# Kernel tuning notes

Hardware: AMD Instinct MI355X
Metric: run time of the kernel (lower is better)

Reference implementation:

```python
import jax, jax.numpy as jnp
import numpy as np

B, N = 16, 512            # graphs, atoms per graph
F_DIM, H, D = 128, 64, 16  # feature_dim, hidden_dim, far_source_dim
CUT, GROWTH = 5.0, 2.0
NS, NT = 3, 2
MULT = GROWTH ** NS        # default far_max_radius_multiplier = 8
EMAX = CUT * MULT          # 40.0
TOT = NS + NT              # 5 shells total
SF = D + 3                 # 19 per-shell features
SE_IN = TOT * SF           # 95
EH_IN = 4 * D + SE_IN      # 159
N_RBF = 8
BOUNDS = [(5.0, 10.0), (10.0, 20.0), (20.0, 40.0), (40.0, 80.0), (80.0, float('inf'))]


def ln(x, g, b):
    m = x.mean(-1, keepdims=True)
    v = x.var(-1, keepdims=True)
    return (x - m) / jnp.sqrt(v + 1e-5) * g + b


def setup_inputs() -> dict:
    key = jax.random.key(0)
    ks = jax.random.split(key, 16)
    W = lambda k, i, o: jax.random.normal(k, (i, o), jnp.float32) / np.sqrt(i)
    inp = {}
    inp['x'] = jax.random.normal(ks[0], (B * N, F_DIM), jnp.float32)
    inp['pos'] = jax.random.uniform(ks[1], (B * N, 3), jnp.float32) * 80.0
    inp['batch'] = jnp.repeat(jnp.arange(B, dtype=jnp.int32), N)
    inp['num_graphs'] = B
    inp['in_ln_g'] = jnp.ones(F_DIM); inp['in_ln_b'] = jnp.zeros(F_DIM)
    inp['src_w1'] = W(ks[2], F_DIM, H); inp['src_b1'] = jnp.zeros(H)
    inp['src_w2'] = W(ks[3], H, D);     inp['src_b2'] = jnp.zeros(D)
    inp['src_ln_g'] = jnp.ones(D); inp['src_ln_b'] = jnp.zeros(D)
    inp['se_ln_g'] = jnp.ones(SE_IN); inp['se_ln_b'] = jnp.zeros(SE_IN)
    inp['se_w1'] = W(ks[4], SE_IN, H); inp['se_b1'] = jnp.zeros(H)
    inp['se_w2'] = W(ks[5], H, D);     inp['se_b2'] = jnp.zeros(D)
    inp['eh_ln_g'] = jnp.ones(EH_IN); inp['eh_ln_b'] = jnp.zeros(EH_IN)
    inp['eh_w1'] = W(ks[6], EH_IN, H); inp['eh_b1'] = jnp.zeros(H)
    inp['eh_w2'] = W(ks[7], H, 1);     inp['eh_b2'] = jnp.zeros(1)
    inp['k_screen'] = jnp.float32(-8.0)
    inp['kg_w1'] = W(ks[8], N_RBF + 2, 32); inp['kg_b1'] = jnp.zeros(32)
    inp['kg_w2'] = jnp.zeros((32, 1)); inp['kg_b2'] = jnp.zeros(1)  # zero-init per source
    inp['far_gate'] = jnp.float32(0.2)
    inp['energy_scale'] = jnp.float32(0.0)
    return inp


def reference(x, pos, batch, num_graphs, in_ln_g, in_ln_b, src_w1, src_b1, src_w2, src_b2,
              src_ln_g, src_ln_b, se_ln_g, se_ln_b, se_w1, se_b1, se_w2, se_b2,
              eh_ln_g, eh_ln_b, eh_w1, eh_b1, eh_w2, eh_b2,
              k_screen, kg_w1, kg_b1, kg_w2, kg_b2, far_gate, energy_scale):
    M = x.shape[0]
    n = M // num_graphs
    # per-atom source features
    h = ln(x, in_ln_g, in_ln_b)
    src = jax.nn.silu(h @ src_w1 + src_b1) @ src_w2 + src_b2
    src = ln(src, src_ln_g, src_ln_b)
    # graph-wise neutralization (subtract per-graph mean)
    gsum = jax.ops.segment_sum(src, batch, num_segments=num_graphs)
    cnt = jax.ops.segment_sum(jnp.ones((M, 1), x.dtype), batch, num_segments=num_graphs)
    src = src - (gsum / jnp.maximum(cnt, 1.0))[batch]
    # pairwise distances per graph
    p = pos.reshape(num_graphs, n, 3)
    s = src.reshape(num_graphs, n, D)
    diff = p[:, :, None, :] - p[:, None, :, :]
    d = jnp.sqrt((diff * diff).sum(-1) + 1e-12)  # [B,n,n]
    not_self = ~jnp.eye(n, dtype=bool)[None]
    # physical kernel with learned RBF gate
    screening = jax.nn.softplus(k_screen)
    base = jnp.exp(-screening * d) / jnp.maximum(d, 1e-6)
    centers = jnp.linspace(CUT, EMAX, N_RBF)
    spacing = (EMAX - CUT) / (N_RBF - 1)
    gamma = 1.0 / (spacing * spacing)
    dc = d[..., None]
    rbf = jnp.exp(-gamma * (dc - centers) ** 2)
    gin = jnp.concatenate([dc / CUT, dc / EMAX, rbf], -1)
    gate = 1.0 + jnp.tanh(jax.nn.silu(gin @ kg_w1 + kg_b1) @ kg_w2 + kg_b2)[..., 0]
    ker = base * gate
    # shell statistics: kernel-weighted mean source, count, mean_r, rms_r per shell
    feats = []
    for lo, up in BOUNDS:
        m = (d >= lo) & not_self
        if np.isfinite(up):
            m = m & (d < up)
        mf = m.astype(x.dtype)
        c = mf.sum(-1)
        denom = jnp.maximum(c, 1.0)
        mean = jnp.einsum('bij,bjc->bic', ker * mf, s) / denom[..., None]
        mr = (mf * d).sum(-1) / denom
        rr = jnp.sqrt((mf * d * d).sum(-1) / denom + 1e-12)
        feats.append(jnp.concatenate([mean, c[..., None], mr[..., None], rr[..., None]], -1))
    shell = jnp.concatenate(feats, -1).reshape(M, SE_IN)  # [M, 95]
    emb = jax.nn.silu(ln(shell, se_ln_g, se_ln_b) @ se_w1 + se_b1) @ se_w2 + se_b2
    ein = jnp.concatenate([src, emb, src * emb, src - emb, shell], -1)  # [M, 159]
    pa = (jax.nn.silu(ln(ein, eh_ln_g, eh_ln_b) @ eh_w1 + eh_b1) @ eh_w2 + eh_b2)[..., 0]
    pa = pa * jnp.tanh(far_gate) * jnp.exp(energy_scale)
    return jax.ops.segment_sum(pa, batch, num_segments=num_graphs)  # per-graph energies [B]
```

## Files before the change

kernel.cpp:

```cpp
#include <hip/hip_runtime.h>
#include <hip/hip_bf16.h>
#include <math.h>

#define B_G   16
#define N_A   512
#define M_AT  8192
#define FD    128
#define HD    64
#define DD    16
#define SEIN  95
#define EHIN  159
#define NLUT  512
#define DMAXF 140.0f

__device__ __forceinline__ float silu_f(float z) { return z / (1.f + __expf(-z)); }

__global__ __launch_bounds__(128) void k_front(
    const float* __restrict__ x,
    const float* __restrict__ g, const float* __restrict__ bb,
    const float* __restrict__ w1, const float* __restrict__ b1,
    const float* __restrict__ w2, const float* __restrict__ b2,
    const float* __restrict__ lng, const float* __restrict__ lnb,
    const float* __restrict__ k_screen,
    const float* __restrict__ kg_w1, const float* __restrict__ kg_b1,
    const float* __restrict__ kg_w2, const float* __restrict__ kg_b2,
    float* __restrict__ srcout, float* __restrict__ partials,
    float2* __restrict__ lut, float* __restrict__ out) {
  int t = threadIdx.x;

  __shared__ __align__(16) float xns[2][FD][5];
  __shared__ __align__(16) float hb[2][HD][5];
  __shared__ float psum[2][16];
  __shared__ float w1l[320], b1l[32], w2l[32];

  if (blockIdx.x >= 1024) {
    int lb = blockIdx.x - 1024;
    if (lb == 0 && t < B_G) out[t] = 0.f;
    for (int idx = t; idx < 320; idx += 128) w1l[idx] = kg_w1[idx];
    if (t < 32) { b1l[t] = kg_b1[t]; w2l[t] = kg_w2[t]; }
    __syncthreads();
    int i = lb * 128 + t;
    float step = DMAXF / (float)(NLUT - 1);
    float ksv = k_screen[0];
    float screening = fmaxf(ksv, 0.f) + log1pf(expf(-fabsf(ksv)));
    float b2v = kg_b2[0];
    float vals[2];
#pragma unroll
    for (int e = 0; e < 2; ++e) {
      int ii = min(i + e, NLUT - 1);
      float d = (float)ii * step;
      float base = expf(-screening * d) / fmaxf(d, 1e-6f);
      float gin[10];
      gin[0] = d * (1.f / 5.0f);
      gin[1] = d * (1.f / 40.0f);
#pragma unroll
      for (int kk = 0; kk < 8; ++kk) {
        float u = d - (5.0f + 5.0f * (float)kk);
        gin[2 + kk] = expf(-(1.f / 25.f) * u * u);
      }
      float accv = 0.f;
      for (int h = 0; h < 32; ++h) {
        float z = b1l[h];
#pragma unroll
        for (int kk = 0; kk < 10; ++kk) z += gin[kk] * w1l[kk * 32 + h];
        accv += silu_f(z) * w2l[h];
      }
      vals[e] = base * (1.f + tanhf(accv + b2v));
    }
    lut[i] = make_float2(vals[0], vals[1] - vals[0]);
    return;
  }

  int wave = t >> 6, lane = t & 63;
  int a = lane >> 4;
  int s = lane & 15;
  int aBase = blockIdx.x * 8 + wave * 4;

  float xr[8];
  {
    const float4* xp = (const float4*)(x + (size_t)(aBase + a) * FD + s * 8);
    float4 v0 = xp[0], v1 = xp[1];
    xr[0]=v0.x; xr[1]=v0.y; xr[2]=v0.z; xr[3]=v0.w;
    xr[4]=v1.x; xr[5]=v1.y; xr[6]=v1.z; xr[7]=v1.w;
  }
  float sm_ = 0.f;
#pragma unroll
  for (int i = 0; i < 8; ++i) sm_ += xr[i];
  sm_ += __shfl_xor(sm_, 1); sm_ += __shfl_xor(sm_, 2);
  sm_ += __shfl_xor(sm_, 4); sm_ += __shfl_xor(sm_, 8);
  float m = sm_ * (1.f / 128.f);
  float v2 = 0.f;
#pragma unroll
  for (int i = 0; i < 8; ++i) { float d = xr[i] - m; v2 += d * d; }
  v2 += __shfl_xor(v2, 1); v2 += __shfl_xor(v2, 2);
  v2 += __shfl_xor(v2, 4); v2 += __shfl_xor(v2, 8);
  float inv = rsqrtf(v2 * (1.f / 128.f) + 1e-5f);
#pragma unroll
  for (int i = 0; i < 8; ++i) {
    int k = s * 8 + i;
    xns[wave][k][a] = (xr[i] - m) * inv * g[k] + bb[k];
  }

  float acc[4] = {0.f, 0.f, 0.f, 0.f};
#pragma unroll 8
  for (int k = 0; k < FD; ++k) {
    float4 wv = ((const float4*)(w1 + (size_t)k * HD))[s];
    float xa = xns[wave][k][a];
    acc[0] += wv.x * xa; acc[1] += wv.y * xa;
    acc[2] += wv.z * xa; acc[3] += wv.w * xa;
  }
  {
    float4 bv = ((const float4*)b1)[s];
    hb[wave][s * 4 + 0][a] = silu_f(acc[0] + bv.x);
    hb[wave][s * 4 + 1][a] = silu_f(acc[1] + bv.y);
    hb[wave][s * 4 + 2][a] = silu_f(acc[2] + bv.z);
    hb[wave][s * 4 + 3][a] = silu_f(acc[3] + bv.w);
  }

  float e = 0.f;
#pragma unroll 8
  for (int k = 0; k < HD; ++k) e += hb[wave][k][a] * w2[k * DD + s];
  float val = e + b2[s];

  float smv = val;
  smv += __shfl_xor(smv, 1); smv += __shfl_xor(smv, 2);
  smv += __shfl_xor(smv, 4); smv += __shfl_xor(smv, 8);
  float mm = smv * (1.f / 16.f);
  float dv = val - mm;
  float vv = dv * dv;
  vv += __shfl_xor(vv, 1); vv += __shfl_xor(vv, 2);
  vv += __shfl_xor(vv, 4); vv += __shfl_xor(vv, 8);
  float iv = rsqrtf(vv * (1.f / 16.f) + 1e-5f);
  float ov = dv * iv * lng[s] + lnb[s];
  srcout[(size_t)(aBase + a) * DD + s] = ov;

  float lsum = ov;
  lsum += __shfl_xor(lsum, 16); lsum += __shfl_xor(lsum, 32);
  if (lane < 16) psum[wave][lane] = lsum;
  __syncthreads();
  if (t < 16) partials[(size_t)blockIdx.x * 16 + t] = psum[0][t] + psum[1][t];
}

__global__ __launch_bounds__(256) void k_pairs_tail(
    const float* __restrict__ pos, const float* __restrict__ src,
    const float2* __restrict__ lut, const float* __restrict__ partials,
    const float* __restrict__ se_ln_g, const float* __restrict__ se_ln_b,
    const float* __restrict__ se_w1, const float* __restrict__ se_b1,
    const float* __restrict__ se_w2, const float* __restrict__ se_b2,
    const float* __restrict__ eh_ln_g, const float* __restrict__ eh_ln_b,
    const float* __restrict__ eh_w1, const float* __restrict__ eh_b1,
    const float* __restrict__ eh_w2, const float* __restrict__ eh_b2,
    const float* __restrict__ far_gate, const float* __restrict__ energy_scale,
    float* __restrict__ out) {
  int gph = blockIdx.x >> 7;
  int blk = blockIdx.x & 127;
  int t = threadIdx.x, wave = t >> 6, lane = t & 63;
  int i_local = blk * 4 + wave;

  __shared__ __align__(16) float sp[N_A * 3];
  __shared__ __align__(16) float ss[N_A * DD];
  __shared__ __align__(16) float2 luts[NLUT];
  __shared__ float smean[16];
  __shared__ __align__(16) float einL[4][160];
  __shared__ __align__(16) float shnL[4][96];
  __shared__ __align__(16) float hbL[4][64];
  __shared__ float redv[4];

  for (int idx = t; idx < N_A * 3 / 4; idx += 256)
    ((float4*)sp)[idx] = ((const float4*)(pos + (size_t)gph * N_A * 3))[idx];
  for (int idx = t; idx < N_A * DD / 4; idx += 256)
    ((float4*)ss)[idx] = ((const float4*)(src + (size_t)gph * N_A * DD))[idx];
  if (t < NLUT / 2) ((float4*)luts)[t] = ((const float4*)lut)[t];
  if (t < 64) {
    int c = t & 15, grp = t >> 4;
    float sm = 0.f;
#pragma unroll
    for (int kk = 0; kk < 16; ++kk)
      sm += partials[(size_t)(gph * 64 + grp * 16 + kk) * 16 + c];
    sm += __shfl_xor(sm, 16); sm += __shfl_xor(sm, 32);
    if (t < 16) smean[c] = sm * (1.f / 512.f);
  }
  __syncthreads();

  int jlow = lane & 15, cq = lane >> 4;
  float px = sp[i_local * 3], py = sp[i_local * 3 + 1], pz = sp[i_local * 3 + 2];
  float accq[5][4] = {};
  float cnt[5] = {0,0,0,0,0}, sdv[5] = {0,0,0,0,0}, sdd[5] = {0,0,0,0,0}, swq[5] = {0,0,0,0,0};
  const float lscale = (float)(NLUT - 1) / DMAXF;

#pragma unroll 8
  for (int jj = 0; jj < 32; ++jj) {
    int j = jj * 16 + jlow;
    float dx = px - sp[j * 3], dy = py - sp[j * 3 + 1], dz = pz - sp[j * 3 + 2];
    float d2 = dx * dx + dy * dy + dz * dz + 1e-12f;
    float d = sqrtf(d2);
    bool valid = (j != i_local) && (d >= 5.0f);
    int tq = (d >= 10.f) + (d >= 20.f) + (d >= 40.f) + (d >= 80.f);
    float xq = d * lscale;
    int i0 = min((int)xq, NLUT - 2);
    float f = xq - (float)i0;
    float2 L = luts[i0];
    float w = valid ? (L.x + L.y * f) : 0.f;
    float dm = valid ? d : 0.f;
    float ddm = valid ? d * d : 0.f;
    float cm = valid ? 1.f : 0.f;
    float4 sv = *(const float4*)&ss[j * DD + cq * 4];
#pragma unroll
    for (int q = 0; q < 5; ++q) {
      bool mq = (tq == q);
      float wq = mq ? w : 0.f;
      accq[q][0] += wq * sv.x; accq[q][1] += wq * sv.y;
      accq[q][2] += wq * sv.z; accq[q][3] += wq * sv.w;
      cnt[q] += mq ? cm : 0.f;
      sdv[q] += mq ? dm : 0.f;
      sdd[q] += mq ? ddm : 0.f;
      swq[q] += wq;
    }
  }
#pragma unroll
  for (int q = 0; q < 5; ++q)
#pragma unroll
    for (int i = 0; i < 4; ++i) {
      float v = accq[q][i];
      v += __shfl_xor(v, 1); v += __shfl_xor(v, 2);
      v += __shfl_xor(v, 4); v += __shfl_xor(v, 8);
      accq[q][i] = v;
    }
#pragma unroll
  for (int q = 0; q < 5; ++q) {
#pragma unroll
    for (int o = 32; o > 0; o >>= 1) {
      cnt[q] += __shfl_xor(cnt[q], o);
      sdv[q] += __shfl_xor(sdv[q], o);
      sdd[q] += __shfl_xor(sdd[q], o);
      swq[q] += __shfl_xor(swq[q], o);
    }
    cnt[q] *= 0.25f; sdv[q] *= 0.25f; sdd[q] *= 0.25f; swq[q] *= 0.25f;
  }

  if (jlow == 0) {
#pragma unroll
    for (int q = 0; q < 5; ++q) {
      float denom = fmaxf(cnt[q], 1.f);
#pragma unroll
      for (int i = 0; i < 4; ++i) {
        int c = cq * 4 + i;
        einL[wave][64 + q * 19 + c] = (accq[q][i] - smean[c] * swq[q]) / denom;
      }
    }
  }
  if (lane < 5) {
    int q = lane;
    float denom = fmaxf(cnt[q], 1.f);
    einL[wave][64 + q * 19 + 16] = cnt[q];
    einL[wave][64 + q * 19 + 17] = sdv[q] / denom;
    einL[wave][64 + q * 19 + 18] = sqrtf(sdd[q] / denom + 1e-12f);
  }

  {
    float v0 = einL[wave][64 + lane];
    float v1 = (lane < 31) ? einL[wave][128 + lane] : 0.f;
    float s1 = v0 + v1, sq = v0 * v0 + v1 * v1;
#pragma unroll
    for (int o = 32; o > 0; o >>= 1) { s1 += __shfl_xor(s1, o); sq += __shfl_xor(sq, o); }
    float mn = s1 * (1.f / (float)SEIN);
    float var = sq * (1.f / (float)SEIN) - mn * mn;
    float invv = rsqrtf(var + 1e-5f);
    shnL[wave][lane] = (v0 - mn) * invv * se_ln_g[lane] + se_ln_b[lane];
    if (lane < 31)
      shnL[wave][64 + lane] = (v1 - mn) * invv * se_ln_g[64 + lane] + se_ln_b[64 + lane];
  }

  {
    float z = se_b1[lane];
#pragma unroll 5
    for (int k = 0; k < SEIN; ++k) z += shnL[wave][k] * se_w1[(size_t)k * HD + lane];
    hbL[wave][lane] = silu_f(z);
  }

  {
    int c = lane & 15, kq = lane >> 4;
    float e = 0.f;
#pragma unroll
    for (int i = 0; i < 16; ++i) {
      int k = kq * 16 + i;
      e += hbL[wave][k] * se_w2[k * DD + c];
    }
    e += __shfl_down(e, 32);
    e += __shfl_down(e, 16);
    if (lane < 16) {
      float ev = e + se_b2[lane];
      float svv = ss[i_local * DD + lane] - smean[lane];
      einL[wave][lane] = svv;
      einL[wave][16 + lane] = ev;
      einL[wave][32 + lane] = svv * ev;
      einL[wave][48 + lane] = svv - ev;
    }
  }

  {
    float u0 = einL[wave][lane];
    float u1 = einL[wave][64 + lane];
    float u2 = (lane < 31) ? einL[wave][128 + lane] : 0.f;
    float s1 = u0 + u1 + u2, sq = u0 * u0 + u1 * u1 + u2 * u2;
#pragma unroll
    for (int o = 32; o > 0; o >>= 1) { s1 += __shfl_xor(s1, o); sq += __shfl_xor(sq, o); }
    float mn = s1 * (1.f / (float)EHIN);
    float var = sq * (1.f / (float)EHIN) - mn * mn;
    float invv = rsqrtf(var + 1e-5f);
    einL[wave][lane] = (u0 - mn) * invv * eh_ln_g[lane] + eh_ln_b[lane];
    einL[wave][64 + lane] = (u1 - mn) * invv * eh_ln_g[64 + lane] + eh_ln_b[64 + lane];
    if (lane < 31)
      einL[wave][128 + lane] = (u2 - mn) * invv * eh_ln_g[128 + lane] + eh_ln_b[128 + lane];
  }

  {
    float z2 = eh_b1[lane];
#pragma unroll 3
    for (int k = 0; k < EHIN; ++k) z2 += einL[wave][k] * eh_w1[(size_t)k * HD + lane];
    float pa = silu_f(z2) * eh_w2[lane];
#pragma unroll
    for (int o = 32; o > 0; o >>= 1) pa += __shfl_xor(pa, o);
    if (lane == 0) redv[wave] = pa + eh_b2[0];
  }
  __syncthreads();
  if (t == 0) {
    float tot = redv[0] + redv[1] + redv[2] + redv[3];
    atomicAdd(&out[gph], tot * tanhf(far_gate[0]) * expf(energy_scale[0]));
  }
}

extern "C" void kernel_launch(void* const* d_in, const int* in_sizes, int n_in,
                              void* d_out, int out_size, void* d_ws, size_t ws_size,
                              hipStream_t stream) {
  const float* x         = (const float*)d_in[0];
  const float* pos       = (const float*)d_in[1];
  const float* in_ln_g   = (const float*)d_in[4];
  const float* in_ln_b   = (const float*)d_in[5];
  const float* src_w1    = (const float*)d_in[6];
  const float* src_b1    = (const float*)d_in[7];
  const float* src_w2    = (const float*)d_in[8];
  const float* src_b2    = (const float*)d_in[9];
  const float* src_ln_g  = (const float*)d_in[10];
  const float* src_ln_b  = (const float*)d_in[11];
  const float* se_ln_g   = (const float*)d_in[12];
  const float* se_ln_b   = (const float*)d_in[13];
  const float* se_w1     = (const float*)d_in[14];
  const float* se_b1     = (const float*)d_in[15];
  const float* se_w2     = (const float*)d_in[16];
  const float* se_b2     = (const float*)d_in[17];
  const float* eh_ln_g   = (const float*)d_in[18];
  const float* eh_ln_b   = (const float*)d_in[19];
  const float* eh_w1     = (const float*)d_in[20];
  const float* eh_b1     = (const float*)d_in[21];
  const float* eh_w2     = (const float*)d_in[22];
  const float* eh_b2     = (const float*)d_in[23];
  const float* k_screen  = (const float*)d_in[24];
  const float* kg_w1     = (const float*)d_in[25];
  const float* kg_b1     = (const float*)d_in[26];
  const float* kg_w2     = (const float*)d_in[27];
  const float* kg_b2     = (const float*)d_in[28];
  const float* far_gate  = (const float*)d_in[29];
  const float* en_scale  = (const float*)d_in[30];
  float* out = (float*)d_out;

  float* ws_src   = (float*)d_ws;
  float* ws_part  = ws_src + (size_t)M_AT * DD;
  float2* ws_lut  = (float2*)(ws_part + 1024 * 16);

  k_front<<<1028, 128, 0, stream>>>(x, in_ln_g, in_ln_b, src_w1, src_b1,
                                    src_w2, src_b2, src_ln_g, src_ln_b,
                                    k_screen, kg_w1, kg_b1, kg_w2, kg_b2,
                                    ws_src, ws_part, ws_lut, out);
  k_pairs_tail<<<B_G * (N_A / 4), 256, 0, stream>>>(
      pos, ws_src, ws_lut, ws_part,
      se_ln_g, se_ln_b, se_w1, se_b1, se_w2, se_b2,
      eh_ln_g, eh_ln_b, eh_w1, eh_b1, eh_w2, eh_b2,
      far_gate, en_scale, out);
}
```

Baseline: 218.0 us.

## Compute pair weights once per lane pair and stage them in shared memory

The pairwise loop used to compute distance, LUT weight and shell index redundantly in every lane of a 4-way channel group. Now each lane handles distinct neighbours, writes the weight and shell index to per-wave shared buffers, and a second pass reads them back to accumulate the weighted source features. This removes the 4x redundant distance and LUT work, at the cost of extra LDS space, LDS traffic and a block barrier. LayerNorm variance is also switched to a two-pass centred form for numerical stability.

```diff
diff --git a/kernel.cpp b/kernel.cpp
--- a/kernel.cpp
+++ b/kernel.cpp
@@ -160,6 +160,8 @@
   __shared__ __align__(16) float sp[N_A * 3];
   __shared__ __align__(16) float ss[N_A * DD];
   __shared__ __align__(16) float2 luts[NLUT];
+  __shared__ __align__(16) float wb[4][N_A];
+  __shared__ unsigned char tbs[4][N_A];
   __shared__ float smean[16];
   __shared__ __align__(16) float einL[4][160];
   __shared__ __align__(16) float shnL[4][96];
@@ -182,39 +184,70 @@
   }
   __syncthreads();
 
-  int jlow = lane & 15, cq = lane >> 4;
   float px = sp[i_local * 3], py = sp[i_local * 3 + 1], pz = sp[i_local * 3 + 2];
-  float accq[5][4] = {};
   float cnt[5] = {0,0,0,0,0}, sdv[5] = {0,0,0,0,0}, sdd[5] = {0,0,0,0,0}, swq[5] = {0,0,0,0,0};
   const float lscale = (float)(NLUT - 1) / DMAXF;
 
-#pragma unroll 8
-  for (int jj = 0; jj < 32; ++jj) {
-    int j = jj * 16 + jlow;
-    float dx = px - sp[j * 3], dy = py - sp[j * 3 + 1], dz = pz - sp[j * 3 + 2];
+#pragma unroll
+  for (int it = 0; it < 8; ++it) {
+    int jv = lane + it * 64;
+    float dx = px - sp[jv * 3], dy = py - sp[jv * 3 + 1], dz = pz - sp[jv * 3 + 2];
     float d2 = dx * dx + dy * dy + dz * dz + 1e-12f;
     float d = sqrtf(d2);
-    bool valid = (j != i_local) && (d >= 5.0f);
+    bool valid = (jv != i_local) && (d >= 5.0f);
     int tq = (d >= 10.f) + (d >= 20.f) + (d >= 40.f) + (d >= 80.f);
     float xq = d * lscale;
     int i0 = min((int)xq, NLUT - 2);
     float f = xq - (float)i0;
     float2 L = luts[i0];
     float w = valid ? (L.x + L.y * f) : 0.f;
+    wb[wave][jv] = w;
+    tbs[wave][jv] = (unsigned char)tq;
     float dm = valid ? d : 0.f;
     float ddm = valid ? d * d : 0.f;
     float cm = valid ? 1.f : 0.f;
-    float4 sv = *(const float4*)&ss[j * DD + cq * 4];
 #pragma unroll
     for (int q = 0; q < 5; ++q) {
       bool mq = (tq == q);
-      float wq = mq ? w : 0.f;
-      accq[q][0] += wq * sv.x; accq[q][1] += wq * sv.y;
-      accq[q][2] += wq * sv.z; accq[q][3] += wq * sv.w;
       cnt[q] += mq ? cm : 0.f;
       sdv[q] += mq ? dm : 0.f;
       sdd[q] += mq ? ddm : 0.f;
-      swq[q] += wq;
+      swq[q] += mq ? w : 0.f;
+    }
+  }
+#pragma unroll
+  for (int q = 0; q < 5; ++q) {
+#pragma unroll
+    for (int o = 32; o > 0; o >>= 1) {
+      cnt[q] += __shfl_xor(cnt[q], o);
+      sdv[q] += __shfl_xor(sdv[q], o);
+      sdd[q] += __shfl_xor(sdd[q], o);
+      swq[q] += __shfl_xor(swq[q], o);
+    }
+  }
+  __syncthreads();
+
+  int jlow = lane & 15, cq = lane >> 4;
+  float accq[5][4] = {};
+  {
+    const float* ssb = &ss[jlow * DD + cq * 4];
+    const float* wbb = &wb[wave][jlow];
+    const unsigned char* tbb = &tbs[wave][jlow];
+#pragma unroll
+    for (int jj = 0; jj < 32; ++jj) {
+      float4 sv = *(const float4*)(ssb + jj * 256);
+      float w = wbb[jj * 16];
+      int tq = tbb[jj * 16];
+      float w0 = (tq == 0) ? w : 0.f;
+      float w1_ = (tq == 1) ? w : 0.f;
+      float w2_ = (tq == 2) ? w : 0.f;
+      float w3_ = (tq == 3) ? w : 0.f;
+      float w4_ = (tq == 4) ? w : 0.f;
+      accq[0][0] += w0 * sv.x; accq[0][1] += w0 * sv.y; accq[0][2] += w0 * sv.z; accq[0][3] += w0 * sv.w;
+      accq[1][0] += w1_ * sv.x; accq[1][1] += w1_ * sv.y; accq[1][2] += w1_ * sv.z; accq[1][3] += w1_ * sv.w;
+      accq[2][0] += w2_ * sv.x; accq[2][1] += w2_ * sv.y; accq[2][2] += w2_ * sv.z; accq[2][3] += w2_ * sv.w;
+      accq[3][0] += w3_ * sv.x; accq[3][1] += w3_ * sv.y; accq[3][2] += w3_ * sv.z; accq[3][3] += w3_ * sv.w;
+      accq[4][0] += w4_ * sv.x; accq[4][1] += w4_ * sv.y; accq[4][2] += w4_ * sv.z; accq[4][3] += w4_ * sv.w;
     }
   }
 #pragma unroll
@@ -226,17 +259,6 @@
       v += __shfl_xor(v, 4); v += __shfl_xor(v, 8);
       accq[q][i] = v;
     }
-#pragma unroll
-  for (int q = 0; q < 5; ++q) {
-#pragma unroll
-    for (int o = 32; o > 0; o >>= 1) {
-      cnt[q] += __shfl_xor(cnt[q], o);
-      sdv[q] += __shfl_xor(sdv[q], o);
-      sdd[q] += __shfl_xor(sdd[q], o);
-      swq[q] += __shfl_xor(swq[q], o);
-    }
-    cnt[q] *= 0.25f; sdv[q] *= 0.25f; sdd[q] *= 0.25f; swq[q] *= 0.25f;
-  }
 
   if (jlow == 0) {
 #pragma unroll
@@ -260,15 +282,18 @@
   {
     float v0 = einL[wave][64 + lane];
     float v1 = (lane < 31) ? einL[wave][128 + lane] : 0.f;
-    float s1 = v0 + v1, sq = v0 * v0 + v1 * v1;
-#pragma unroll
-    for (int o = 32; o > 0; o >>= 1) { s1 += __shfl_xor(s1, o); sq += __shfl_xor(sq, o); }
+    float s1 = v0 + v1;
+#pragma unroll
+    for (int o = 32; o > 0; o >>= 1) s1 += __shfl_xor(s1, o);
     float mn = s1 * (1.f / (float)SEIN);
-    float var = sq * (1.f / (float)SEIN) - mn * mn;
-    float invv = rsqrtf(var + 1e-5f);
-    shnL[wave][lane] = (v0 - mn) * invv * se_ln_g[lane] + se_ln_b[lane];
+    float d0 = v0 - mn, d1 = (lane < 31) ? v1 - mn : 0.f;
+    float sq = d0 * d0 + d1 * d1;
+#pragma unroll
+    for (int o = 32; o > 0; o >>= 1) sq += __shfl_xor(sq, o);
+    float invv = rsqrtf(sq * (1.f / (float)SEIN) + 1e-5f);
+    shnL[wave][lane] = d0 * invv * se_ln_g[lane] + se_ln_b[lane];
     if (lane < 31)
-      shnL[wave][64 + lane] = (v1 - mn) * invv * se_ln_g[64 + lane] + se_ln_b[64 + lane];
+      shnL[wave][64 + lane] = d1 * invv * se_ln_g[64 + lane] + se_ln_b[64 + lane];
   }
 
   {
@@ -302,16 +327,19 @@
     float u0 = einL[wave][lane];
     float u1 = einL[wave][64 + lane];
     float u2 = (lane < 31) ? einL[wave][128 + lane] : 0.f;
-    float s1 = u0 + u1 + u2, sq = u0 * u0 + u1 * u1 + u2 * u2;
-#pragma unroll
-    for (int o = 32; o > 0; o >>= 1) { s1 += __shfl_xor(s1, o); sq += __shfl_xor(sq, o); }
+    float s1 = u0 + u1 + u2;
+#pragma unroll
+    for (int o = 32; o > 0; o >>= 1) s1 += __shfl_xor(s1, o);
     float mn = s1 * (1.f / (float)EHIN);
-    float var = sq * (1.f / (float)EHIN) - mn * mn;
-    float invv = rsqrtf(var + 1e-5f);
-    einL[wave][lane] = (u0 - mn) * invv * eh_ln_g[lane] + eh_ln_b[lane];
-    einL[wave][64 + lane] = (u1 - mn) * invv * eh_ln_g[64 + lane] + eh_ln_b[64 + lane];
+    float e0 = u0 - mn, e1 = u1 - mn, e2 = (lane < 31) ? u2 - mn : 0.f;
+    float sq = e0 * e0 + e1 * e1 + e2 * e2;
+#pragma unroll
+    for (int o = 32; o > 0; o >>= 1) sq += __shfl_xor(sq, o);
+    float invv = rsqrtf(sq * (1.f / (float)EHIN) + 1e-5f);
+    einL[wave][lane] = e0 * invv * eh_ln_g[lane] + eh_ln_b[lane];
+    einL[wave][64 + lane] = e1 * invv * eh_ln_g[64 + lane] + eh_ln_b[64 + lane];
     if (lane < 31)
-      einL[wave][128 + lane] = (u2 - mn) * invv * eh_ln_g[128 + lane] + eh_ln_b[128 + lane];
+      einL[wave][128 + lane] = e2 * invv * eh_ln_g[128 + lane] + eh_ln_b[128 + lane];
   }
 
   {
```

Result: slower. 230.0 us (+5.5%).
